# Kernel optimization log

Hardware: AMD Instinct MI355X
Metric: run time of the kernel (lower is better)

Reference implementation:

```python
import jax, jax.numpy as jnp
import numpy as np

BN_EPS = 1e-5


def binarize(x):
    # sign binarization with straight-through estimator (identity grad)
    return x + jax.lax.stop_gradient(jnp.sign(x) - x)


def conv2d(x, w, stride):
    # x: [N,C,H,W], w: [O,I,kh,kw], VALID padding (PyTorch default padding=0)
    return jax.lax.conv_general_dilated(
        x, w, window_strides=(stride, stride), padding='VALID',
        dimension_numbers=('NCHW', 'OIHW', 'NCHW'))


def batchnorm(x, gamma, beta, mean, var):
    inv = gamma / jnp.sqrt(var + BN_EPS)          # [C]
    return x * inv[None, :, None, None] + (beta - mean * inv)[None, :, None, None]


def setup_inputs() -> dict:
    key = jax.random.key(0)
    ks = jax.random.split(key, 20)
    B = 8192
    f32 = jnp.float32
    d = {
        'x': jax.random.normal(ks[0], (B, 1, 24, 54), f32),
        'conv1_w': jax.random.normal(ks[1], (32, 1, 3, 3), f32) * 0.3,
        'conv1_b': jax.random.normal(ks[2], (32,), f32) * 0.1,
        'bn1_gamma': 1.0 + 0.1 * jax.random.normal(ks[3], (32,), f32),
        'bn1_beta': 0.1 * jax.random.normal(ks[4], (32,), f32),
        'bn1_mean': 0.1 * jax.random.normal(ks[5], (32,), f32),
        'bn1_var': jax.random.uniform(ks[6], (32,), f32, 0.5, 1.5),
        'conv2_w': jax.random.normal(ks[7], (64, 32, 3, 3), f32) * 0.1,
        'conv2_b': jax.random.normal(ks[8], (64,), f32) * 0.1,
        'bn2_gamma': 1.0 + 0.1 * jax.random.normal(ks[9], (64,), f32),
        'bn2_beta': 0.1 * jax.random.normal(ks[10], (64,), f32),
        'bn2_mean': 0.1 * jax.random.normal(ks[11], (64,), f32),
        'bn2_var': jax.random.uniform(ks[12], (64,), f32, 0.5, 1.5),
        'lin_w': jax.random.normal(ks[13], (500, 3840), f32) * 0.02,
        'lin_b': jax.random.normal(ks[14], (500,), f32) * 0.1,
        'out_w': jax.random.normal(ks[15], (10, 500), f32) * 0.05,
        'out_b': jax.random.normal(ks[16], (10,), f32) * 0.1,
    }
    return d


def reference(x, conv1_w, conv1_b, bn1_gamma, bn1_beta, bn1_mean, bn1_var,
              conv2_w, conv2_b, bn2_gamma, bn2_beta, bn2_mean, bn2_var,
              lin_w, lin_b, out_w, out_b):
    # conv1: input channels (1) != 3 -> input binarized; weight binarized; float bias
    h = conv2d(binarize(x), binarize(conv1_w), 2) + conv1_b[None, :, None, None]
    h = jax.nn.relu(batchnorm(h, bn1_gamma, bn1_beta, bn1_mean, bn1_var))  # [B,32,11,26]
    # conv2: input channels (32) != 3 -> input binarized (values in {0,1} post-ReLU)
    h = conv2d(binarize(h), binarize(conv2_w), 2) + conv2_b[None, :, None, None]
    h = jax.nn.relu(batchnorm(h, bn2_gamma, bn2_beta, bn2_mean, bn2_var))  # [B,64,5,12]
    h = h.reshape(-1, 3840)
    # BinarizeLinear: in_features (3840, 500) != 784 -> input binarized
    h = jax.nn.relu(binarize(h) @ binarize(lin_w).T + lin_b[None, :])      # [B,500]
    y = binarize(h) @ binarize(out_w).T + out_b[None, :]                   # [B,10]
    return y
```

## Files before the change

kernel.cpp:

```cpp
#include <hip/hip_runtime.h>
#include <cstdint>

#define BN_EPS 1e-5f

static constexpr int NB = 8192;
static constexpr int JLIN = 500;

typedef int v4i  __attribute__((ext_vector_type(4)));
typedef int v16i __attribute__((ext_vector_type(16)));


__global__ __launch_bounds__(256) void pack_kernel(
    const float* __restrict__ conv1_w, const float* __restrict__ conv1_b,
    const float* __restrict__ conv2_w, const float* __restrict__ conv2_b,
    const float* __restrict__ lin_w, const float* __restrict__ lin_b,
    const float* __restrict__ out_w,
    const float* __restrict__ bn1_g, const float* __restrict__ bn1_b,
    const float* __restrict__ bn1_m, const float* __restrict__ bn1_v,
    const float* __restrict__ bn2_g, const float* __restrict__ bn2_b,
    const float* __restrict__ bn2_m, const float* __restrict__ bn2_v,
    uint4* __restrict__ wbfrag, uint32_t* __restrict__ cdat,
    uint32_t* __restrict__ lut, uint32_t* __restrict__ wout,
    int* __restrict__ Tlin, uint4* __restrict__ wcfrag)
{
    __shared__ float    s_c1w[288];
    __shared__ uint32_t s_wp[32];
    __shared__ float    s_inv1[32], s_sh1[32], s_b1[32];

    int tid = threadIdx.x;
    int b   = blockIdx.x;

    if (b < 512) {
        int e  = b * 256 + tid;
        int L  = e & 63;
        int kq = (e >> 6) & 127;
        int jt = e >> 13;
        int j  = jt * 32 + (L & 31);
        int h  = L >> 5;
        uint32_t dd[4] = {0u, 0u, 0u, 0u};
        if (j < JLIN) {
            int c  = kq >> 1, hi = kq & 1;
            int nb = (hi ? 28 : 32) - 16 * h;
            const float4* s4 = (const float4*)(lin_w + (size_t)j * 3840 +
                                               c * 60 + hi * 32 + 16 * h);
            float4 q0 = s4[0], q1 = s4[1], q2 = s4[2], q3 = s4[3];
            float qf[16] = {q0.x, q0.y, q0.z, q0.w, q1.x, q1.y, q1.z, q1.w,
                            q2.x, q2.y, q2.z, q2.w, q3.x, q3.y, q3.z, q3.w};
            #pragma unroll
            for (int i = 0; i < 16; ++i) {
                uint32_t byte = (i < nb) ? ((qf[i] > 0.0f) ? 0x01u : 0xFFu) : 0u;
                dd[i >> 2] |= byte << (8 * (i & 3));
            }
        }
        wbfrag[e] = make_uint4(dd[0], dd[1], dd[2], dd[3]);
        return;
    }

    if (b >= 520) {
        int e = (b - 520) * 256 + tid;
        if (e < 1152) {
            int t = e >> 7;
            int n = (e >> 6) & 1;
            int L = e & 63;
            int c = n * 32 + (L & 31);
            int hb = L >> 5;
            bool flip = (bn2_g[c] < 0.0f);
            uint32_t dd[4] = {0u, 0u, 0u, 0u};
            #pragma unroll
            for (int i = 0; i < 16; ++i) {
                int ic = 16 * hb + i;
                float w = conv2_w[c * 288 + ic * 9 + t];
                uint32_t byte = ((w > 0.0f) == flip) ? 0xFFu : 0x01u;
                dd[i >> 2] |= byte << (8 * (i & 3));
            }
            wcfrag[e] = make_uint4(dd[0], dd[1], dd[2], dd[3]);
        }
        return;
    }

    int mb = b - 512;
    if (mb < 2) {
        for (int i = tid; i < 288; i += 256) s_c1w[i] = conv1_w[i];
        __syncthreads();
        if (tid < 32) {
            uint32_t wp = 0;
            for (int t = 0; t < 9; ++t)
                wp |= (s_c1w[tid * 9 + t] < 0.0f ? 1u : 0u) << t;
            s_wp[tid] = wp;
            float inv = bn1_g[tid] / sqrtf(bn1_v[tid] + BN_EPS);
            s_inv1[tid] = inv;
            s_sh1[tid]  = bn1_b[tid] - bn1_m[tid] * inv;
            s_b1[tid]   = conv1_b[tid];
        }
        __syncthreads();
        uint32_t px = (uint32_t)(mb * 256 + tid);
        uint32_t word = 0;
        for (int c = 0; c < 32; ++c) {
            int d = 9 - 2 * __popc(px ^ s_wp[c]);
            float z = __fadd_rn((float)d, s_b1[c]);
            z = __fadd_rn(__fmul_rn(z, s_inv1[c]), s_sh1[c]);
            word |= (z > 0.0f ? 1u : 0u) << c;
        }
        lut[px] = word;
        return;
    }

    int idx = (mb - 2) * 256 + tid;
    if (idx < 576) {
        int c = idx / 9, tap = idx % 9;
        uint32_t w = 0;
        for (int ic = 0; ic < 32; ++ic)
            w |= (conv2_w[c * 288 + ic * 9 + tap] > 0.0f ? 1u : 0u) << ic;
        float inv = bn2_g[c] / sqrtf(bn2_v[c] + BN_EPS);
        if (inv < 0.0f) w = ~w;
        cdat[tap * 64 + c] = w;
    } else if (idx < 576 + 64) {
        int c = idx - 576;
        float inv = bn2_g[c] / sqrtf(bn2_v[c] + BN_EPS);
        float sh  = bn2_b[c] - bn2_m[c] * inv;
        float b2  = conv2_b[c];
        int T = 10000;
        for (int u = -300; u <= 300; ++u) {
            float v = (inv < 0.0f) ? (float)(-u) : (float)u;
            float z = __fadd_rn(__fmul_rn(__fadd_rn(v, b2), inv), sh);
            if (z > 0.0f) { T = u; break; }
        }
        cdat[576 + c] = (uint32_t)T;
    } else if (idx < 576 + 64 + 512) {
        int j = idx - (576 + 64);
        int T = 10000;
        if (j < JLIN) {
            float lb = lin_b[j];
            int base = (int)floorf(-lb) - 2;
            for (int u = base; u <= base + 5; ++u)
                if (__fadd_rn((float)u, lb) > 0.0f) { T = u; break; }
        }
        Tlin[j] = T;
    } else if (idx < 576 + 64 + 512 + 160) {
        int t = idx - (576 + 64 + 512);
        int j = t >> 4, k = t & 15;
        uint32_t w = 0;
        for (int bb = 0; bb < 32; ++bb) {
            int jj = k * 32 + bb;
            if (jj < JLIN) w |= (out_w[j * 500 + jj] > 0.0f ? 1u : 0u) << bb;
        }
        wout[t] = w;
    }
}

__global__ __launch_bounds__(256) void conv_kernel(
    const float* __restrict__ x,
    const uint32_t* __restrict__ cdat,
    const uint32_t* __restrict__ lut,
    const uint4* __restrict__ wcfrag,
    uint32_t* __restrict__ h2b)
{
    __shared__ uint32_t s_lut[512];
    __shared__ __align__(8) uint32_t s_flat[4][44];
    __shared__ uint32_t s_words[4][288];

    int tid  = threadIdx.x;
    int lane = tid & 63;
    int wv   = tid >> 6;
    int s    = blockIdx.x * 4 + wv;

    s_lut[tid]       = lut[tid];
    s_lut[tid + 256] = lut[tid + 256];
    __syncthreads();

    const float* xs = x + (size_t)s * 1296;
    float xv[21];
    #pragma unroll
    for (int it = 0; it < 21; ++it) {
        int f = it * 64 + lane;
        xv[it] = (f < 1296) ? xs[f] : 1.0f;
    }
    #pragma unroll
    for (int it = 0; it < 21; ++it) {
        uint64_t mk = __ballot(xv[it] < 0.0f);
        if (lane == 0) *(uint64_t*)&s_flat[wv][2 * it] = mk;
    }
    asm volatile("s_waitcnt lgkmcnt(0)" ::: "memory");
    __builtin_amdgcn_sched_barrier(0);

    #pragma unroll
    for (int ii = 0; ii < 5; ++ii) {
        int wnd = ii * 64 + lane;
        if (wnd < 286) {
            int oy = wnd / 26, ox = wnd - 26 * oy;
            uint32_t pxb = 0;
            #pragma unroll
            for (int ky = 0; ky < 3; ++ky) {
                int bitpos = 54 * (2 * oy + ky) + 2 * ox;
                int d = bitpos >> 5, sh = bitpos & 31;
                uint64_t wp = (uint64_t)s_flat[wv][d] |
                              ((uint64_t)s_flat[wv][d + 1] << 32);
                pxb |= (((uint32_t)(wp >> sh)) & 7u) << (3 * ky);
            }
            s_words[wv][wnd] = s_lut[pxb];
        }
    }
    asm volatile("s_waitcnt lgkmcnt(0)" ::: "memory");
    __builtin_amdgcn_sched_barrier(0);

    int row32 = lane & 31;
    int hb    = lane >> 5;
    int sh_hb = 16 * hb;
    int p1v   = 32 + row32; if (p1v > 59) p1v = 59;
    int wb0, wb1;
    { int oy = row32 / 12, ox = row32 - 12 * oy; wb0 = 52 * oy + 2 * ox; }
    { int oy = p1v / 12,   ox = p1v - 12 * oy;   wb1 = 52 * oy + 2 * ox; }

    v16i acc[2][2] = {};
    #pragma unroll
    for (int t = 0; t < 9; ++t) {
        const int koff = (t / 3) * 26 + (t % 3);
        uint4 b0 = wcfrag[t * 128 + lane];
        uint4 b1 = wcfrag[t * 128 + 64 + lane];
        v4i bf0 = {(int)b0.x, (int)b0.y, (int)b0.z, (int)b0.w};
        v4i bf1 = {(int)b1.x, (int)b1.y, (int)b1.z, (int)b1.w};
        #pragma unroll
        for (int rt = 0; rt < 2; ++rt) {
            uint32_t w  = s_words[wv][(rt ? wb1 : wb0) + koff];
            uint32_t hw = w >> sh_hb;
            v4i af;
            af[0] = (int)((((hw      ) & 0xFu) * 0x204081u) & 0x01010101u);
            af[1] = (int)((((hw >> 4 ) & 0xFu) * 0x204081u) & 0x01010101u);
            af[2] = (int)((((hw >> 8 ) & 0xFu) * 0x204081u) & 0x01010101u);
            af[3] = (int)((((hw >> 12) & 0xFu) * 0x204081u) & 0x01010101u);
            acc[rt][0] = __builtin_amdgcn_mfma_i32_32x32x32_i8(af, bf0, acc[rt][0], 0, 0, 0);
            acc[rt][1] = __builtin_amdgcn_mfma_i32_32x32x32_i8(af, bf1, acc[rt][1], 0, 0, 0);
        }
    }

    {
        int T0 = (int)cdat[576 + row32];
        int T1 = (int)cdat[576 + 32 + row32];
        uint32_t w_rt[2];
        #pragma unroll
        for (int rt = 0; rt < 2; ++rt) {
            uint32_t lw0 = 0, lw1 = 0;
            #pragma unroll
            for (int r = 0; r < 16; ++r) {
                const uint32_t pb = 1u << ((r & 3) + 8 * (r >> 2));
                if (acc[rt][0][r] >= T0) lw0 |= pb;
                if (acc[rt][1][r] >= T1) lw1 |= pb;
            }
            lw0 <<= 4 * hb;
            lw1 <<= 4 * hb;
            uint32_t send = hb ? lw0 : lw1;
            uint32_t recv = (uint32_t)__shfl_xor((int)send, 32);
            w_rt[rt] = recv | (hb ? lw1 : lw0);
        }
        uint32_t w0 = w_rt[0];
        uint32_t w1 = w_rt[1] & 0x0FFFFFFFu;
        *(uint2*)(h2b + (size_t)s * 128 + 2 * lane) = make_uint2(w0, w1);
    }
}

__global__ __launch_bounds__(256) void lin2_kernel(
    const uint32_t* __restrict__ h2b,
    const uint4* __restrict__ wbfrag,
    const int* __restrict__ Tlin,
    uint32_t* __restrict__ h3w)
{
    __shared__ uint8_t As[64 * 520];

    int tid  = threadIdx.x;
    int lane = tid & 63;
    int wv   = __builtin_amdgcn_readfirstlane((int)(tid >> 6));
    int sblk = blockIdx.x >> 3;
    int jgrp = blockIdx.x & 7;
    int jt   = jgrp * 2 + (wv >> 1);
    int roff = (wv & 1) * 32;
    int s0   = sblk * 64;

    int T = Tlin[jt * 32 + (lane & 31)];
    int row  = roff + (lane & 31);
    int half = lane >> 5;

    v16i acc = {};
    uint32_t wreg[4];
    #pragma unroll
    for (int ii = 0; ii < 4; ++ii) {
        int e = ii * 256 + tid;
        wreg[ii] = h2b[(size_t)(s0 + (e >> 4)) * 128 + (e & 15)];
    }

    for (int chunk = 0; chunk < 8; ++chunk) {
        #pragma unroll
        for (int ii = 0; ii < 4; ++ii) {
            int e = ii * 256 + tid;
            int smx = e >> 4, wlx = e & 15;
            uint32_t w = wreg[ii];
            uint32_t dw[8];
            #pragma unroll
            for (int q = 0; q < 8; ++q)
                dw[q] = (((w >> (4 * q)) & 0xFu) * 0x204081u) & 0x01010101u;
            uint64_t* dst = (uint64_t*)(As + smx * 520 + wlx * 32);
            dst[0] = (uint64_t)dw[0] | ((uint64_t)dw[1] << 32);
            dst[1] = (uint64_t)dw[2] | ((uint64_t)dw[3] << 32);
            dst[2] = (uint64_t)dw[4] | ((uint64_t)dw[5] << 32);
            dst[3] = (uint64_t)dw[6] | ((uint64_t)dw[7] << 32);
        }
        __syncthreads();

        if (chunk < 7) {
            #pragma unroll
            for (int ii = 0; ii < 4; ++ii) {
                int e = ii * 256 + tid;
                wreg[ii] = h2b[(size_t)(s0 + (e >> 4)) * 128 +
                               (chunk + 1) * 16 + (e & 15)];
            }
        }

        const uint4* bsrc = wbfrag + ((size_t)jt * 128 + chunk * 16) * 64 + lane;
        #pragma unroll 4
        for (int kq = 0; kq < 16; ++kq) {
            uint4 bw = bsrc[kq * 64];
            v4i bf = {(int)bw.x, (int)bw.y, (int)bw.z, (int)bw.w};
            const uint8_t* ap = As + row * 520 + kq * 32 + half * 16;
            uint64_t lo0 = *(const uint64_t*)ap;
            uint64_t hi0 = *(const uint64_t*)(ap + 8);
            v4i a0 = {(int)(uint32_t)lo0, (int)(lo0 >> 32),
                      (int)(uint32_t)hi0, (int)(hi0 >> 32)};
            acc = __builtin_amdgcn_mfma_i32_32x32x32_i8(a0, bf, acc, 0, 0, 0);
        }
        __syncthreads();
    }

    #pragma unroll
    for (int r = 0; r < 16; ++r) {
        int row0 = (r & 3) + 8 * (r >> 2);
        uint64_t mk = __ballot(acc[r] >= T);
        if (lane == 0) {
            h3w[(size_t)(s0 + roff + row0) * 16 + jt]     = (uint32_t)mk;
            h3w[(size_t)(s0 + roff + row0 + 4) * 16 + jt] = (uint32_t)(mk >> 32);
        }
    }
}

__global__ __launch_bounds__(64) void out_kernel(
    const uint32_t* __restrict__ h3w,
    const uint32_t* __restrict__ wout,
    const float* __restrict__ out_b,
    float* __restrict__ out)
{
    int s = blockIdx.x * 64 + threadIdx.x;
    const uint4* hp = (const uint4*)(h3w + (size_t)s * 16);
    uint4 q0 = hp[0], q1 = hp[1], q2 = hp[2], q3 = hp[3];
    uint32_t w[16] = {q0.x, q0.y, q0.z, q0.w, q1.x, q1.y, q1.z, q1.w,
                      q2.x, q2.y, q2.z, q2.w, q3.x, q3.y, q3.z, q3.w};
    int B = 0;
    #pragma unroll
    for (int k = 0; k < 16; ++k) B += __popc(w[k]);
    #pragma unroll
    for (int o = 0; o < 10; ++o) {
        int P = 0;
        #pragma unroll
        for (int k = 0; k < 16; ++k) P += __popc(w[k] & wout[o * 16 + k]);
        out[(size_t)s * 10 + o] = __fadd_rn((float)(2 * P - B), out_b[o]);
    }
}

extern "C" void kernel_launch(void* const* d_in, const int* in_sizes, int n_in,
                              void* d_out, int out_size, void* d_ws, size_t ws_size,
                              hipStream_t stream)
{
    const float* x       = (const float*)d_in[0];
    const float* conv1_w = (const float*)d_in[1];
    const float* conv1_b = (const float*)d_in[2];
    const float* bn1_g   = (const float*)d_in[3];
    const float* bn1_b   = (const float*)d_in[4];
    const float* bn1_m   = (const float*)d_in[5];
    const float* bn1_v   = (const float*)d_in[6];
    const float* conv2_w = (const float*)d_in[7];
    const float* conv2_b = (const float*)d_in[8];
    const float* bn2_g   = (const float*)d_in[9];
    const float* bn2_b   = (const float*)d_in[10];
    const float* bn2_m   = (const float*)d_in[11];
    const float* bn2_v   = (const float*)d_in[12];
    const float* lin_w   = (const float*)d_in[13];
    const float* lin_b   = (const float*)d_in[14];
    const float* out_w   = (const float*)d_in[15];
    const float* out_b   = (const float*)d_in[16];

    char* ws = (char*)d_ws;
    uint32_t* h2b    = (uint32_t*)(ws + 0);
    uint4*    wbfrag = (uint4*)   (ws + 4194304);
    uint32_t* h3w    = (uint32_t*)(ws + 6291456);
    uint32_t* cdat   = (uint32_t*)(ws + 6815744);
    uint32_t* lut    = (uint32_t*)(ws + 6818304);
    uint32_t* wout   = (uint32_t*)(ws + 6820352);
    int*      Tlin   = (int*)     (ws + 6820992);
    uint4*    wcfrag = (uint4*)   (ws + 6855808);

    pack_kernel<<<525, 256, 0, stream>>>(conv1_w, conv1_b, conv2_w, conv2_b,
                                         lin_w, lin_b, out_w,
                                         bn1_g, bn1_b, bn1_m, bn1_v,
                                         bn2_g, bn2_b, bn2_m, bn2_v,
                                         wbfrag, cdat, lut, wout, Tlin, wcfrag);
    conv_kernel<<<NB / 4, 256, 0, stream>>>(x, cdat, lut, wcfrag, h2b);
    lin2_kernel<<<1024, 256, 0, stream>>>(h2b, wbfrag, Tlin, h3w);
    out_kernel<<<128, 64, 0, stream>>>(h3w, wout, out_b, (float*)d_out);
}
```

Baseline: 166.6 us.

## Drop LDS staging in lin2 and expand binarized activations in registers

The binary linear kernel no longer stages expanded activation bytes in shared memory with block barriers. Each wave now loads its 32 sample rows of packed bits directly from global memory and expands nibbles to int8 per MFMA in registers. The work mapping changes so each block handles one output tile for 128 samples across 4 waves. This removes LDS writes and reads and syncthreads, at the cost of redundant global loads of activations and weight fragments per wave.

```diff
diff --git a/kernel.cpp b/kernel.cpp
--- a/kernel.cpp
+++ b/kernel.cpp
@@ -264,69 +264,42 @@
     const int* __restrict__ Tlin,
     uint32_t* __restrict__ h3w)
 {
-    __shared__ uint8_t As[64 * 520];
-
-    int tid  = threadIdx.x;
-    int lane = tid & 63;
-    int wv   = __builtin_amdgcn_readfirstlane((int)(tid >> 6));
-    int sblk = blockIdx.x >> 3;
-    int jgrp = blockIdx.x & 7;
-    int jt   = jgrp * 2 + (wv >> 1);
-    int roff = (wv & 1) * 32;
-    int s0   = sblk * 64;
-
-    int T = Tlin[jt * 32 + (lane & 31)];
-    int row  = roff + (lane & 31);
-    int half = lane >> 5;
+    int tid   = threadIdx.x;
+    int lane  = tid & 63;
+    int wv    = tid >> 6;
+    int jt    = blockIdx.x & 15;
+    int sgrp  = (blockIdx.x >> 4) * 4 + wv;
+    int sbase = sgrp * 32;
+    int half  = lane >> 5;
+    int r32   = lane & 31;
+    int shh   = 16 * half;
+
+    int T = Tlin[jt * 32 + r32];
+    const uint4* arow  = (const uint4*)(h2b + (size_t)(sbase + r32) * 128);
+    const uint4* bbase = wbfrag + (size_t)jt * 128 * 64 + lane;
 
     v16i acc = {};
-    uint32_t wreg[4];
-    #pragma unroll
-    for (int ii = 0; ii < 4; ++ii) {
-        int e = ii * 256 + tid;
-        wreg[ii] = h2b[(size_t)(s0 + (e >> 4)) * 128 + (e & 15)];
-    }
-
     for (int chunk = 0; chunk < 8; ++chunk) {
-        #pragma unroll
-        for (int ii = 0; ii < 4; ++ii) {
-            int e = ii * 256 + tid;
-            int smx = e >> 4, wlx = e & 15;
-            uint32_t w = wreg[ii];
-            uint32_t dw[8];
-            #pragma unroll
-            for (int q = 0; q < 8; ++q)
-                dw[q] = (((w >> (4 * q)) & 0xFu) * 0x204081u) & 0x01010101u;
-            uint64_t* dst = (uint64_t*)(As + smx * 520 + wlx * 32);
-            dst[0] = (uint64_t)dw[0] | ((uint64_t)dw[1] << 32);
-            dst[1] = (uint64_t)dw[2] | ((uint64_t)dw[3] << 32);
-            dst[2] = (uint64_t)dw[4] | ((uint64_t)dw[5] << 32);
-            dst[3] = (uint64_t)dw[6] | ((uint64_t)dw[7] << 32);
-        }
-        __syncthreads();
-
-        if (chunk < 7) {
-            #pragma unroll
-            for (int ii = 0; ii < 4; ++ii) {
-                int e = ii * 256 + tid;
-                wreg[ii] = h2b[(size_t)(s0 + (e >> 4)) * 128 +
-                               (chunk + 1) * 16 + (e & 15)];
-            }
-        }
-
-        const uint4* bsrc = wbfrag + ((size_t)jt * 128 + chunk * 16) * 64 + lane;
-        #pragma unroll 4
+        uint4 w4[4];
+        #pragma unroll
+        for (int i = 0; i < 4; ++i) w4[i] = arow[chunk * 4 + i];
+        uint32_t wq[16] = {w4[0].x, w4[0].y, w4[0].z, w4[0].w,
+                           w4[1].x, w4[1].y, w4[1].z, w4[1].w,
+                           w4[2].x, w4[2].y, w4[2].z, w4[2].w,
+                           w4[3].x, w4[3].y, w4[3].z, w4[3].w};
+        const uint4* bsrc = bbase + (size_t)(chunk * 16) * 64;
+        #pragma unroll
         for (int kq = 0; kq < 16; ++kq) {
             uint4 bw = bsrc[kq * 64];
             v4i bf = {(int)bw.x, (int)bw.y, (int)bw.z, (int)bw.w};
-            const uint8_t* ap = As + row * 520 + kq * 32 + half * 16;
-            uint64_t lo0 = *(const uint64_t*)ap;
-            uint64_t hi0 = *(const uint64_t*)(ap + 8);
-            v4i a0 = {(int)(uint32_t)lo0, (int)(lo0 >> 32),
-                      (int)(uint32_t)hi0, (int)(hi0 >> 32)};
-            acc = __builtin_amdgcn_mfma_i32_32x32x32_i8(a0, bf, acc, 0, 0, 0);
-        }
-        __syncthreads();
+            uint32_t hw = wq[kq] >> shh;
+            v4i af;
+            af[0] = (int)((((hw      ) & 0xFu) * 0x204081u) & 0x01010101u);
+            af[1] = (int)((((hw >> 4 ) & 0xFu) * 0x204081u) & 0x01010101u);
+            af[2] = (int)((((hw >> 8 ) & 0xFu) * 0x204081u) & 0x01010101u);
+            af[3] = (int)((((hw >> 12) & 0xFu) * 0x204081u) & 0x01010101u);
+            acc = __builtin_amdgcn_mfma_i32_32x32x32_i8(af, bf, acc, 0, 0, 0);
+        }
     }
 
     #pragma unroll
@@ -334,8 +307,8 @@
         int row0 = (r & 3) + 8 * (r >> 2);
         uint64_t mk = __ballot(acc[r] >= T);
         if (lane == 0) {
-            h3w[(size_t)(s0 + roff + row0) * 16 + jt]     = (uint32_t)mk;
-            h3w[(size_t)(s0 + roff + row0 + 4) * 16 + jt] = (uint32_t)(mk >> 32);
+            h3w[(size_t)(sbase + row0) * 16 + jt]     = (uint32_t)mk;
+            h3w[(size_t)(sbase + row0 + 4) * 16 + jt] = (uint32_t)(mk >> 32);
         }
     }
 }
```

Result: no change. 168.4 us (+1.1%).

## Fuse conv, binary linear and output layers into one kernel

Applied to the files above, without the earlier changes.

Merges the conv, lin2 and out kernels into one kernel with 512 threads per block, each block handling 32 samples. Conv outputs and hidden bits stay in LDS instead of going through global memory, and two launches are removed. In exchange, each block now streams the full packed linear weights for only 32 rows, roughly doubling total weight traffic through L2. Only 256 blocks are launched, which lowers occupancy and latency hiding.

```diff
diff --git a/kernel.cpp b/kernel.cpp
--- a/kernel.cpp
+++ b/kernel.cpp
@@ -148,60 +148,33 @@
     }
 }
 
-__global__ __launch_bounds__(256) void conv_kernel(
+__global__ __launch_bounds__(512) void fused_kernel(
     const float* __restrict__ x,
     const uint32_t* __restrict__ cdat,
     const uint32_t* __restrict__ lut,
     const uint4* __restrict__ wcfrag,
-    uint32_t* __restrict__ h2b)
+    const uint4* __restrict__ wbfrag,
+    const int* __restrict__ Tlin,
+    const uint32_t* __restrict__ wout,
+    const float* __restrict__ out_b,
+    float* __restrict__ out)
 {
     __shared__ uint32_t s_lut[512];
-    __shared__ __align__(8) uint32_t s_flat[4][44];
-    __shared__ uint32_t s_words[4][288];
+    __shared__ uint32_t s_wout[160];
+    __shared__ __align__(8) uint32_t s_flat[8][44];
+    __shared__ uint32_t s_words[8][288];
+    __shared__ __align__(8) uint32_t h2w[32][130];
+    __shared__ __align__(16) uint8_t As[32 * 520];
+    __shared__ uint32_t s_h3[32][16];
 
     int tid  = threadIdx.x;
     int lane = tid & 63;
     int wv   = tid >> 6;
-    int s    = blockIdx.x * 4 + wv;
-
-    s_lut[tid]       = lut[tid];
-    s_lut[tid + 256] = lut[tid + 256];
+    int blk  = blockIdx.x;
+
+    s_lut[tid] = lut[tid];
+    if (tid < 160) s_wout[tid] = wout[tid];
     __syncthreads();
-
-    const float* xs = x + (size_t)s * 1296;
-    float xv[21];
-    #pragma unroll
-    for (int it = 0; it < 21; ++it) {
-        int f = it * 64 + lane;
-        xv[it] = (f < 1296) ? xs[f] : 1.0f;
-    }
-    #pragma unroll
-    for (int it = 0; it < 21; ++it) {
-        uint64_t mk = __ballot(xv[it] < 0.0f);
-        if (lane == 0) *(uint64_t*)&s_flat[wv][2 * it] = mk;
-    }
-    asm volatile("s_waitcnt lgkmcnt(0)" ::: "memory");
-    __builtin_amdgcn_sched_barrier(0);
-
-    #pragma unroll
-    for (int ii = 0; ii < 5; ++ii) {
-        int wnd = ii * 64 + lane;
-        if (wnd < 286) {
-            int oy = wnd / 26, ox = wnd - 26 * oy;
-            uint32_t pxb = 0;
-            #pragma unroll
-            for (int ky = 0; ky < 3; ++ky) {
-                int bitpos = 54 * (2 * oy + ky) + 2 * ox;
-                int d = bitpos >> 5, sh = bitpos & 31;
-                uint64_t wp = (uint64_t)s_flat[wv][d] |
-                              ((uint64_t)s_flat[wv][d + 1] << 32);
-                pxb |= (((uint32_t)(wp >> sh)) & 7u) << (3 * ky);
-            }
-            s_words[wv][wnd] = s_lut[pxb];
-        }
-    }
-    asm volatile("s_waitcnt lgkmcnt(0)" ::: "memory");
-    __builtin_amdgcn_sched_barrier(0);
 
     int row32 = lane & 31;
     int hb    = lane >> 5;
@@ -210,89 +183,104 @@
     int wb0, wb1;
     { int oy = row32 / 12, ox = row32 - 12 * oy; wb0 = 52 * oy + 2 * ox; }
     { int oy = p1v / 12,   ox = p1v - 12 * oy;   wb1 = 52 * oy + 2 * ox; }
-
-    v16i acc[2][2] = {};
-    #pragma unroll
-    for (int t = 0; t < 9; ++t) {
-        const int koff = (t / 3) * 26 + (t % 3);
-        uint4 b0 = wcfrag[t * 128 + lane];
-        uint4 b1 = wcfrag[t * 128 + 64 + lane];
-        v4i bf0 = {(int)b0.x, (int)b0.y, (int)b0.z, (int)b0.w};
-        v4i bf1 = {(int)b1.x, (int)b1.y, (int)b1.z, (int)b1.w};
-        #pragma unroll
-        for (int rt = 0; rt < 2; ++rt) {
-            uint32_t w  = s_words[wv][(rt ? wb1 : wb0) + koff];
-            uint32_t hw = w >> sh_hb;
-            v4i af;
-            af[0] = (int)((((hw      ) & 0xFu) * 0x204081u) & 0x01010101u);
-            af[1] = (int)((((hw >> 4 ) & 0xFu) * 0x204081u) & 0x01010101u);
-            af[2] = (int)((((hw >> 8 ) & 0xFu) * 0x204081u) & 0x01010101u);
-            af[3] = (int)((((hw >> 12) & 0xFu) * 0x204081u) & 0x01010101u);
-            acc[rt][0] = __builtin_amdgcn_mfma_i32_32x32x32_i8(af, bf0, acc[rt][0], 0, 0, 0);
-            acc[rt][1] = __builtin_amdgcn_mfma_i32_32x32x32_i8(af, bf1, acc[rt][1], 0, 0, 0);
-        }
-    }
-
-    {
-        int T0 = (int)cdat[576 + row32];
-        int T1 = (int)cdat[576 + 32 + row32];
-        uint32_t w_rt[2];
-        #pragma unroll
-        for (int rt = 0; rt < 2; ++rt) {
-            uint32_t lw0 = 0, lw1 = 0;
-            #pragma unroll
-            for (int r = 0; r < 16; ++r) {
-                const uint32_t pb = 1u << ((r & 3) + 8 * (r >> 2));
-                if (acc[rt][0][r] >= T0) lw0 |= pb;
-                if (acc[rt][1][r] >= T1) lw1 |= pb;
-            }
-            lw0 <<= 4 * hb;
-            lw1 <<= 4 * hb;
-            uint32_t send = hb ? lw0 : lw1;
-            uint32_t recv = (uint32_t)__shfl_xor((int)send, 32);
-            w_rt[rt] = recv | (hb ? lw1 : lw0);
-        }
-        uint32_t w0 = w_rt[0];
-        uint32_t w1 = w_rt[1] & 0x0FFFFFFFu;
-        *(uint2*)(h2b + (size_t)s * 128 + 2 * lane) = make_uint2(w0, w1);
-    }
-}
-
-__global__ __launch_bounds__(256) void lin2_kernel(
-    const uint32_t* __restrict__ h2b,
-    const uint4* __restrict__ wbfrag,
-    const int* __restrict__ Tlin,
-    uint32_t* __restrict__ h3w)
-{
-    __shared__ uint8_t As[64 * 520];
-
-    int tid  = threadIdx.x;
-    int lane = tid & 63;
-    int wv   = __builtin_amdgcn_readfirstlane((int)(tid >> 6));
-    int sblk = blockIdx.x >> 3;
-    int jgrp = blockIdx.x & 7;
-    int jt   = jgrp * 2 + (wv >> 1);
-    int roff = (wv & 1) * 32;
-    int s0   = sblk * 64;
-
-    int T = Tlin[jt * 32 + (lane & 31)];
-    int row  = roff + (lane & 31);
-    int half = lane >> 5;
-
-    v16i acc = {};
-    uint32_t wreg[4];
-    #pragma unroll
-    for (int ii = 0; ii < 4; ++ii) {
-        int e = ii * 256 + tid;
-        wreg[ii] = h2b[(size_t)(s0 + (e >> 4)) * 128 + (e & 15)];
-    }
+    int T0 = (int)cdat[576 + row32];
+    int T1 = (int)cdat[576 + 32 + row32];
+
+    for (int i = 0; i < 4; ++i) {
+        int sl = wv * 4 + i;
+        const float* xs = x + ((size_t)blk * 32 + sl) * 1296;
+
+        float xv[21];
+        #pragma unroll
+        for (int it = 0; it < 21; ++it) {
+            int f = it * 64 + lane;
+            xv[it] = (f < 1296) ? xs[f] : 1.0f;
+        }
+        #pragma unroll
+        for (int it = 0; it < 21; ++it) {
+            uint64_t mk = __ballot(xv[it] < 0.0f);
+            if (lane == 0) *(uint64_t*)&s_flat[wv][2 * it] = mk;
+        }
+        asm volatile("s_waitcnt lgkmcnt(0)" ::: "memory");
+        __builtin_amdgcn_sched_barrier(0);
+
+        #pragma unroll
+        for (int ii = 0; ii < 5; ++ii) {
+            int wnd = ii * 64 + lane;
+            if (wnd < 286) {
+                int oy = wnd / 26, ox = wnd - 26 * oy;
+                uint32_t pxb = 0;
+                #pragma unroll
+                for (int ky = 0; ky < 3; ++ky) {
+                    int bitpos = 54 * (2 * oy + ky) + 2 * ox;
+                    int d = bitpos >> 5, sh = bitpos & 31;
+                    uint64_t wp = (uint64_t)s_flat[wv][d] |
+                                  ((uint64_t)s_flat[wv][d + 1] << 32);
+                    pxb |= (((uint32_t)(wp >> sh)) & 7u) << (3 * ky);
+                }
+                s_words[wv][wnd] = s_lut[pxb];
+            }
+        }
+        asm volatile("s_waitcnt lgkmcnt(0)" ::: "memory");
+        __builtin_amdgcn_sched_barrier(0);
+
+        v16i acc[2][2] = {};
+        #pragma unroll
+        for (int t = 0; t < 9; ++t) {
+            const int koff = (t / 3) * 26 + (t % 3);
+            uint4 b0 = wcfrag[t * 128 + lane];
+            uint4 b1 = wcfrag[t * 128 + 64 + lane];
+            v4i bf0 = {(int)b0.x, (int)b0.y, (int)b0.z, (int)b0.w};
+            v4i bf1 = {(int)b1.x, (int)b1.y, (int)b1.z, (int)b1.w};
+            #pragma unroll
+            for (int rt = 0; rt < 2; ++rt) {
+                uint32_t w  = s_words[wv][(rt ? wb1 : wb0) + koff];
+                uint32_t hw = w >> sh_hb;
+                v4i af;
+                af[0] = (int)((((hw      ) & 0xFu) * 0x204081u) & 0x01010101u);
+                af[1] = (int)((((hw >> 4 ) & 0xFu) * 0x204081u) & 0x01010101u);
+                af[2] = (int)((((hw >> 8 ) & 0xFu) * 0x204081u) & 0x01010101u);
+                af[3] = (int)((((hw >> 12) & 0xFu) * 0x204081u) & 0x01010101u);
+                acc[rt][0] = __builtin_amdgcn_mfma_i32_32x32x32_i8(af, bf0, acc[rt][0], 0, 0, 0);
+                acc[rt][1] = __builtin_amdgcn_mfma_i32_32x32x32_i8(af, bf1, acc[rt][1], 0, 0, 0);
+            }
+        }
+
+        {
+            uint32_t w_rt[2];
+            #pragma unroll
+            for (int rt = 0; rt < 2; ++rt) {
+                uint32_t lw0 = 0, lw1 = 0;
+                #pragma unroll
+                for (int r = 0; r < 16; ++r) {
+                    const uint32_t pb = 1u << ((r & 3) + 8 * (r >> 2));
+                    if (acc[rt][0][r] >= T0) lw0 |= pb;
+                    if (acc[rt][1][r] >= T1) lw1 |= pb;
+                }
+                lw0 <<= 4 * hb;
+                lw1 <<= 4 * hb;
+                uint32_t send = hb ? lw0 : lw1;
+                uint32_t recv = (uint32_t)__shfl_xor((int)send, 32);
+                w_rt[rt] = recv | (hb ? lw1 : lw0);
+            }
+            uint32_t w0 = w_rt[0];
+            uint32_t w1 = w_rt[1] & 0x0FFFFFFFu;
+            *(uint2*)&h2w[sl][2 * lane] = make_uint2(w0, w1);
+        }
+    }
+    __syncthreads();
+
+    int jt0 = wv, jt1 = wv + 8;
+    int Ta = Tlin[jt0 * 32 + row32];
+    int Tb = Tlin[jt1 * 32 + row32];
+    int smx = tid >> 4, wlx = tid & 15;
+
+    v16i acc0 = {};
+    v16i acc1 = {};
 
     for (int chunk = 0; chunk < 8; ++chunk) {
-        #pragma unroll
-        for (int ii = 0; ii < 4; ++ii) {
-            int e = ii * 256 + tid;
-            int smx = e >> 4, wlx = e & 15;
-            uint32_t w = wreg[ii];
+        {
+            uint32_t w = h2w[smx][chunk * 16 + wlx];
             uint32_t dw[8];
             #pragma unroll
             for (int q = 0; q < 8; ++q)
@@ -305,26 +293,21 @@
         }
         __syncthreads();
 
-        if (chunk < 7) {
-            #pragma unroll
-            for (int ii = 0; ii < 4; ++ii) {
-                int e = ii * 256 + tid;
-                wreg[ii] = h2b[(size_t)(s0 + (e >> 4)) * 128 +
-                               (chunk + 1) * 16 + (e & 15)];
-            }
-        }
-
-        const uint4* bsrc = wbfrag + ((size_t)jt * 128 + chunk * 16) * 64 + lane;
+        const uint4* b0p = wbfrag + ((size_t)jt0 * 128 + chunk * 16) * 64 + lane;
+        const uint4* b1p = wbfrag + ((size_t)jt1 * 128 + chunk * 16) * 64 + lane;
         #pragma unroll 4
         for (int kq = 0; kq < 16; ++kq) {
-            uint4 bw = bsrc[kq * 64];
-            v4i bf = {(int)bw.x, (int)bw.y, (int)bw.z, (int)bw.w};
-            const uint8_t* ap = As + row * 520 + kq * 32 + half * 16;
+            uint4 bw0 = b0p[kq * 64];
+            uint4 bw1 = b1p[kq * 64];
+            v4i bf0 = {(int)bw0.x, (int)bw0.y, (int)bw0.z, (int)bw0.w};
+            v4i bf1 = {(int)bw1.x, (int)bw1.y, (int)bw1.z, (int)bw1.w};
+            const uint8_t* ap = As + row32 * 520 + kq * 32 + hb * 16;
             uint64_t lo0 = *(const uint64_t*)ap;
             uint64_t hi0 = *(const uint64_t*)(ap + 8);
             v4i a0 = {(int)(uint32_t)lo0, (int)(lo0 >> 32),
                       (int)(uint32_t)hi0, (int)(hi0 >> 32)};
-            acc = __builtin_amdgcn_mfma_i32_32x32x32_i8(a0, bf, acc, 0, 0, 0);
+            acc0 = __builtin_amdgcn_mfma_i32_32x32x32_i8(a0, bf0, acc0, 0, 0, 0);
+            acc1 = __builtin_amdgcn_mfma_i32_32x32x32_i8(a0, bf1, acc1, 0, 0, 0);
         }
         __syncthreads();
     }
@@ -332,34 +315,27 @@
     #pragma unroll
     for (int r = 0; r < 16; ++r) {
         int row0 = (r & 3) + 8 * (r >> 2);
-        uint64_t mk = __ballot(acc[r] >= T);
+        uint64_t mk0 = __ballot(acc0[r] >= Ta);
+        uint64_t mk1 = __ballot(acc1[r] >= Tb);
         if (lane == 0) {
-            h3w[(size_t)(s0 + roff + row0) * 16 + jt]     = (uint32_t)mk;
-            h3w[(size_t)(s0 + roff + row0 + 4) * 16 + jt] = (uint32_t)(mk >> 32);
-        }
-    }
-}
-
-__global__ __launch_bounds__(64) void out_kernel(
-    const uint32_t* __restrict__ h3w,
-    const uint32_t* __restrict__ wout,
-    const float* __restrict__ out_b,
-    float* __restrict__ out)
-{
-    int s = blockIdx.x * 64 + threadIdx.x;
-    const uint4* hp = (const uint4*)(h3w + (size_t)s * 16);
-    uint4 q0 = hp[0], q1 = hp[1], q2 = hp[2], q3 = hp[3];
-    uint32_t w[16] = {q0.x, q0.y, q0.z, q0.w, q1.x, q1.y, q1.z, q1.w,
-                      q2.x, q2.y, q2.z, q2.w, q3.x, q3.y, q3.z, q3.w};
-    int B = 0;
-    #pragma unroll
-    for (int k = 0; k < 16; ++k) B += __popc(w[k]);
-    #pragma unroll
-    for (int o = 0; o < 10; ++o) {
-        int P = 0;
-        #pragma unroll
-        for (int k = 0; k < 16; ++k) P += __popc(w[k] & wout[o * 16 + k]);
-        out[(size_t)s * 10 + o] = __fadd_rn((float)(2 * P - B), out_b[o]);
+            s_h3[row0][jt0]     = (uint32_t)mk0;
+            s_h3[row0 + 4][jt0] = (uint32_t)(mk0 >> 32);
+            s_h3[row0][jt1]     = (uint32_t)mk1;
+            s_h3[row0 + 4][jt1] = (uint32_t)(mk1 >> 32);
+        }
+    }
+    __syncthreads();
+
+    if (tid < 320) {
+        int sl = tid / 10, o = tid - 10 * sl;
+        int B = 0, P = 0;
+        #pragma unroll
+        for (int k = 0; k < 16; ++k) {
+            uint32_t w = s_h3[sl][k];
+            B += __popc(w);
+            P += __popc(w & s_wout[o * 16 + k]);
+        }
+        out[((size_t)blk * 32 + sl) * 10 + o] = __fadd_rn((float)(2 * P - B), out_b[o]);
     }
 }
 
@@ -386,9 +362,7 @@
     const float* out_b   = (const float*)d_in[16];
 
     char* ws = (char*)d_ws;
-    uint32_t* h2b    = (uint32_t*)(ws + 0);
     uint4*    wbfrag = (uint4*)   (ws + 4194304);
-    uint32_t* h3w    = (uint32_t*)(ws + 6291456);
     uint32_t* cdat   = (uint32_t*)(ws + 6815744);
     uint32_t* lut    = (uint32_t*)(ws + 6818304);
     uint32_t* wout   = (uint32_t*)(ws + 6820352);
@@ -400,7 +374,6 @@
                                          bn1_g, bn1_b, bn1_m, bn1_v,
                                          bn2_g, bn2_b, bn2_m, bn2_v,
                                          wbfrag, cdat, lut, wout, Tlin, wcfrag);
-    conv_kernel<<<NB / 4, 256, 0, stream>>>(x, cdat, lut, wcfrag, h2b);
-    lin2_kernel<<<1024, 256, 0, stream>>>(h2b, wbfrag, Tlin, h3w);
-    out_kernel<<<128, 64, 0, stream>>>(h3w, wout, out_b, (float*)d_out);
+    fused_kernel<<<256, 512, 0, stream>>>(x, cdat, lut, wcfrag, wbfrag,
+                                          Tlin, wout, out_b, (float*)d_out);
 }
```

Result: no change. 165.6 us (-0.6%).
